# Kernel optimization log

Measured on AMD Instinct MI355X. Metric: run time of the kernel, lower is better.

Reference implementation:

```python
import jax, jax.numpy as jnp
import numpy as np

B, LQ, LK, D, H = 4, 2048, 2048, 1024, 16
HD = D // H  # head dim = 64


def setup_inputs() -> dict:
    key = jax.random.key(0)
    ks = jax.random.split(key, 8)
    s = 1.0 / np.sqrt(D)
    return {
        "zt": jax.random.normal(ks[0], (B, LQ, D), jnp.float32),
        "ic": jax.random.normal(ks[1], (B, LK, D), jnp.float32),
        "Wq": jax.random.normal(ks[2], (D, D), jnp.float32) * s,
        "bq": jax.random.normal(ks[3], (D,), jnp.float32) * 0.01,
        "Wk": jax.random.normal(ks[4], (D, D), jnp.float32) * s,
        "bk": jax.random.normal(ks[5], (D,), jnp.float32) * 0.01,
        "Wv": jax.random.normal(ks[6], (D, D), jnp.float32) * s,
        "bv": jax.random.normal(ks[7], (D,), jnp.float32) * 0.01,
    }


def reference(zt, ic, Wq, bq, Wk, bk, Wv, bv):
    # Linear projections (torch Linear: x @ W.T + b); weights here stored as [out, in]
    q = zt @ Wq.T + bq            # [B, LQ, D]
    k = ic @ Wk.T + bk            # [B, LK, D]
    v = ic @ Wv.T + bv            # [B, LK, D]
    # split heads -> [B, H, L, HD]
    q = q.reshape(B, LQ, H, HD).transpose(0, 2, 1, 3)
    k = k.reshape(B, LK, H, HD).transpose(0, 2, 1, 3)
    v = v.reshape(B, LK, H, HD).transpose(0, 2, 1, 3)
    scale = 1.0 / jnp.sqrt(jnp.asarray(HD, q.dtype))
    scores = jnp.einsum('bhqd,bhkd->bhqk', q, k) * scale  # [B, H, LQ, LK]
    attn = jax.nn.softmax(scores, axis=-1)
    out = jnp.einsum('bhqk,bhkd->bhqd', attn, v)          # [B, H, LQ, HD]
    return out.transpose(0, 2, 1, 3).reshape(B, LQ, D)
```

## Files before the change

kernel.cpp:

```cpp
#include <hip/hip_runtime.h>
#include <hip/hip_bf16.h>
#include <cstdint>

#define B_  4
#define LQ_ 2048
#define LK_ 2048
#define D_  1024
#define H_  16
#define HD_ 64

typedef __attribute__((ext_vector_type(8))) short bf16x8;
typedef __attribute__((ext_vector_type(4))) float f32x4;

#if defined(__has_builtin)
#if __has_builtin(__builtin_amdgcn_exp2f)
#define EXP2F(x) __builtin_amdgcn_exp2f(x)
#else
#define EXP2F(x) exp2f(x)
#endif
#else
#define EXP2F(x) exp2f(x)
#endif

__device__ __forceinline__ unsigned short f2b(float f) {
    union { float f; unsigned u; } v; v.f = f;
    unsigned u = v.u;
    unsigned r = (u + 0x7fffu + ((u >> 16) & 1u)) >> 16;
    return (unsigned short)r;
}

__device__ __forceinline__ void gl_lds16(const unsigned short* g, unsigned short* l) {
    __builtin_amdgcn_global_load_lds(
        (const __attribute__((address_space(1))) unsigned int*)(g),
        (__attribute__((address_space(3))) unsigned int*)(l),
        16, 0, 0);
}

#define PHASE_BARRIER() do { \
    __builtin_amdgcn_sched_barrier(0); \
    __builtin_amdgcn_s_barrier(); \
    __builtin_amdgcn_sched_barrier(0); } while (0)

#define WAITVM(N) do { \
    asm volatile("s_waitcnt vmcnt(" #N ")" ::: "memory"); \
    __builtin_amdgcn_sched_barrier(0); } while (0)

__global__ void cvt_all(const float* __restrict__ a0, unsigned short* __restrict__ d0,
                        const float* __restrict__ a1, unsigned short* __restrict__ d1,
                        const float* __restrict__ w0, unsigned short* __restrict__ e0, float s0,
                        const float* __restrict__ w1, unsigned short* __restrict__ e1,
                        const float* __restrict__ w2, unsigned short* __restrict__ e2,
                        int nact, int nw) {
    const float* in; unsigned short* out; float s = 1.0f; int n;
    switch (blockIdx.y) {
        case 0: in = a0; out = d0; n = nact; break;
        case 1: in = a1; out = d1; n = nact; break;
        case 2: in = w0; out = e0; n = nw; s = s0; break;
        case 3: in = w1; out = e1; n = nw; break;
        default: in = w2; out = e2; n = nw; break;
    }
    int i = (blockIdx.x * blockDim.x + threadIdx.x) * 8;
    int stride = gridDim.x * blockDim.x * 8;
    for (; i < n; i += stride) {
        float4 x = *(const float4*)(in + i);
        float4 y = *(const float4*)(in + i + 4);
        bf16x8 v;
        v[0] = (short)f2b(x.x * s); v[1] = (short)f2b(x.y * s);
        v[2] = (short)f2b(x.z * s); v[3] = (short)f2b(x.w * s);
        v[4] = (short)f2b(y.x * s); v[5] = (short)f2b(y.y * s);
        v[6] = (short)f2b(y.z * s); v[7] = (short)f2b(y.w * s);
        *(bf16x8*)(out + i) = v;
    }
}

__global__ __launch_bounds__(512, 2) void qkv_gemm(
    const unsigned short* __restrict__ Xq,
    const unsigned short* __restrict__ Xkv,
    const unsigned short* __restrict__ Wqb, const unsigned short* __restrict__ Wkb,
    const unsigned short* __restrict__ Wvb,
    const float* __restrict__ bq, const float* __restrict__ bk,
    const float* __restrict__ bv, float qscale,
    unsigned short* __restrict__ Qb, unsigned short* __restrict__ Kb,
    unsigned short* __restrict__ Vtb)
{
    __shared__ unsigned short AS[4][8192];
    __shared__ unsigned short BS[4][8192];

    const int proj = blockIdx.y >> 2;
    const int nt0  = blockIdx.y & 3;
    const unsigned short* X = (proj == 0) ? Xq : Xkv;
    const unsigned short* W = (proj == 0) ? Wqb : (proj == 1 ? Wkb : Wvb);
    const float* bias       = (proj == 0) ? bq  : (proj == 1 ? bk  : bv);
    const float bscale      = (proj == 0) ? qscale : 1.0f;

    const int tid  = threadIdx.x;
    const int lane = tid & 63;
    const int w    = tid >> 6;
    const int wm   = w & 1, wn = w >> 1;
    const int m0   = blockIdx.x * 256;
    const int n0   = nt0 * 256;
    const int l15  = lane & 15, quad = lane >> 4;

    f32x4 acc[8][4] = {};

    const unsigned short* gA0 = X + (size_t)(m0 + (w * 2) * 16 + l15) * 1024 + quad * 8;
    const unsigned short* gA1 = gA0 + 16 * 1024;
    const unsigned short* gB0 = W + (size_t)(n0 + (w * 2) * 16 + l15) * 1024 + quad * 8;
    const unsigned short* gB1 = gB0 + 16 * 1024;

#define STAGE_A(slot, koff) do { \
    gl_lds16(gA0 + (koff), &AS[slot][(w * 2) * 512 + lane * 8]); \
    gl_lds16(gA1 + (koff), &AS[slot][(w * 2 + 1) * 512 + lane * 8]); } while (0)
#define STAGE_B(slot, koff) do { \
    gl_lds16(gB0 + (koff), &BS[slot][(w * 2) * 512 + lane * 8]); \
    gl_lds16(gB1 + (koff), &BS[slot][(w * 2 + 1) * 512 + lane * 8]); } while (0)

    const int aoff = (wm * 8) * 512 + lane * 8;
    const int boff = (wn * 4) * 512 + lane * 8;

    STAGE_A(0, 0);   STAGE_B(0, 0);
    STAGE_A(1, 32);  STAGE_B(1, 32);
    STAGE_A(2, 64);  STAGE_B(2, 64);
    WAITVM(8);
    __builtin_amdgcn_s_barrier();
    __builtin_amdgcn_sched_barrier(0);

    #pragma unroll 2
    for (int t = 0; t < 16; ++t) {
        const int s0 = (2 * t) & 3;
        const int s1 = (2 * t + 1) & 3;
        const int s3 = (2 * t + 3) & 3;

        bf16x8 af[8], bf0, bf1;

        #pragma unroll
        for (int i = 0; i < 8; ++i)
            af[i] = *(const bf16x8*)(&AS[s0][aoff + i * 512]);
        bf0 = *(const bf16x8*)(&BS[s0][boff]);
        bf1 = *(const bf16x8*)(&BS[s0][boff + 512]);
        PHASE_BARRIER();
        __builtin_amdgcn_s_setprio(1);
        #pragma unroll
        for (int i = 0; i < 8; ++i) {
            acc[i][0] = __builtin_amdgcn_mfma_f32_16x16x32_bf16(af[i], bf0, acc[i][0], 0, 0, 0);
            acc[i][1] = __builtin_amdgcn_mfma_f32_16x16x32_bf16(af[i], bf1, acc[i][1], 0, 0, 0);
        }
        __builtin_amdgcn_s_setprio(0);
        if (t < 15) STAGE_A(s3, (t + 1) * 64 + 32);

        bf0 = *(const bf16x8*)(&BS[s0][boff + 1024]);
        bf1 = *(const bf16x8*)(&BS[s0][boff + 1536]);
        if (t < 14) { WAITVM(6); } else { WAITVM(0); }
        PHASE_BARRIER();
        __builtin_amdgcn_s_setprio(1);
        #pragma unroll
        for (int i = 0; i < 8; ++i) {
            acc[i][2] = __builtin_amdgcn_mfma_f32_16x16x32_bf16(af[i], bf0, acc[i][2], 0, 0, 0);
            acc[i][3] = __builtin_amdgcn_mfma_f32_16x16x32_bf16(af[i], bf1, acc[i][3], 0, 0, 0);
        }
        __builtin_amdgcn_s_setprio(0);
        if (t < 15) STAGE_B(s3, (t + 1) * 64 + 32);

        #pragma unroll
        for (int i = 0; i < 8; ++i)
            af[i] = *(const bf16x8*)(&AS[s1][aoff + i * 512]);
        bf0 = *(const bf16x8*)(&BS[s1][boff]);
        bf1 = *(const bf16x8*)(&BS[s1][boff + 512]);
        PHASE_BARRIER();
        __builtin_amdgcn_s_setprio(1);
        #pragma unroll
        for (int i = 0; i < 8; ++i) {
            acc[i][0] = __builtin_amdgcn_mfma_f32_16x16x32_bf16(af[i], bf0, acc[i][0], 0, 0, 0);
            acc[i][1] = __builtin_amdgcn_mfma_f32_16x16x32_bf16(af[i], bf1, acc[i][1], 0, 0, 0);
        }
        __builtin_amdgcn_s_setprio(0);
        if (t < 14) STAGE_A(s0, (t + 2) * 64);

        bf0 = *(const bf16x8*)(&BS[s1][boff + 1024]);
        bf1 = *(const bf16x8*)(&BS[s1][boff + 1536]);
        if (t < 14) { WAITVM(6); } else if (t == 14) { WAITVM(4); }
        PHASE_BARRIER();
        __builtin_amdgcn_s_setprio(1);
        #pragma unroll
        for (int i = 0; i < 8; ++i) {
            acc[i][2] = __builtin_amdgcn_mfma_f32_16x16x32_bf16(af[i], bf0, acc[i][2], 0, 0, 0);
            acc[i][3] = __builtin_amdgcn_mfma_f32_16x16x32_bf16(af[i], bf1, acc[i][3], 0, 0, 0);
        }
        __builtin_amdgcn_s_setprio(0);
        if (t < 14) STAGE_B(s0, (t + 2) * 64);
    }

#undef STAGE_A
#undef STAGE_B

    float bvv[4];
    #pragma unroll
    for (int j = 0; j < 4; ++j)
        bvv[j] = bias[n0 + wn * 64 + j * 16 + l15] * bscale;

    if (proj == 2) {
        #pragma unroll
        for (int i = 0; i < 8; ++i) {
            int row = m0 + wm * 128 + i * 16 + quad * 4;
            int bb  = row >> 11;
            int tt  = row & 2047;
            #pragma unroll
            for (int j = 0; j < 4; ++j) {
                int col = n0 + wn * 64 + j * 16 + l15;
                unsigned s0v = f2b(acc[i][j][0] + bvv[j]);
                unsigned s1v = f2b(acc[i][j][1] + bvv[j]);
                unsigned s2v = f2b(acc[i][j][2] + bvv[j]);
                unsigned s3v = f2b(acc[i][j][3] + bvv[j]);
                uint2 pk;
                pk.x = s0v | (s1v << 16);
                pk.y = s2v | (s3v << 16);
                *(uint2*)(Vtb + ((size_t)(bb * 1024 + col)) * 2048 + tt) = pk;
            }
        }
    } else {
        unsigned short* Y = (proj == 0) ? Qb : Kb;
        #pragma unroll
        for (int i = 0; i < 8; ++i) {
            #pragma unroll
            for (int r = 0; r < 4; ++r) {
                int row = m0 + wm * 128 + i * 16 + quad * 4 + r;
                unsigned short* yp = Y + (size_t)row * 1024 + n0 + wn * 64;
                #pragma unroll
                for (int j = 0; j < 4; ++j)
                    yp[j * 16 + l15] = f2b(acc[i][j][r] + bvv[j]);
            }
        }
    }
}

__global__ __launch_bounds__(256, 2) void attn_kernel(
    const unsigned short* __restrict__ Q,
    const unsigned short* __restrict__ Kp,
    const unsigned short* __restrict__ Vt,
    float* __restrict__ Out)
{
    __shared__ unsigned short Ks[2][16 * 512];
    __shared__ unsigned short Vs[16 * 512];
    __shared__ unsigned short Ps[4][4096];

    const int tid  = threadIdx.x;
    const int lane = tid & 63;
    const int w    = tid >> 6;
    const int l15  = lane & 15, quad = lane >> 4;

    const int bid = blockIdx.x + (blockIdx.y << 3) + (blockIdx.z << 7);
    const int glo = bid & 7;
    const int jx  = bid >> 3;
    const int qt  = jx & 7;
    const int g   = glo + ((jx >> 3) << 3);
    const int h   = g & 15;
    const int b   = g >> 4;

    bf16x8 qf[4][2];
    #pragma unroll
    for (int half = 0; half < 4; ++half) {
        const unsigned short* qptr =
            Q + (size_t)(b * LQ_ + qt * 256 + w * 64 + half * 16 + l15) * 1024 + h * 64;
        qf[half][0] = *(const bf16x8*)(qptr + quad * 8);
        qf[half][1] = *(const bf16x8*)(qptr + 32 + quad * 8);
    }

    bf16x8 ones;
    #pragma unroll
    for (int j = 0; j < 8; ++j) ones[j] = (short)0x3F80;

    f32x4 oacc[4][4] = {};
    f32x4 lacc[4]    = {};

    const unsigned short* Kbase = Kp + (size_t)b * LK_ * 1024 + h * 64;
    const unsigned short* Vbase = Vt + (size_t)(b * 16 + h) * 64 * 2048;

    const unsigned short* gK[4];
    unsigned short* lK[4];
    const unsigned short* gV[4];
    unsigned short* lV[4];
    #pragma unroll
    for (int j = 0; j < 4; ++j) {
        int kt = w + (j >> 1) * 4, dblk = j & 1;
        gK[j] = Kbase + (size_t)(kt * 16 + l15) * 1024 + dblk * 32 + quad * 8;
        lK[j] = &Ks[0][(kt * 2 + dblk) * 512 + lane * 8];
        gV[j] = Vbase + (size_t)(w * 16 + l15) * 2048 + j * 32 + quad * 8;
        lV[j] = &Vs[(w * 4 + j) * 512 + lane * 8];
    }

    const int pws = (quad >> 1) * 128 + l15 * 8 + (quad & 1) * 4;
    unsigned short* PwB = &Ps[w][pws];
    const unsigned short* PrB = &Ps[w][lane * 8];
    const unsigned short* KfrB = &Ks[0][lane * 8];
    const unsigned short* Vfr = &Vs[lane * 8];

    #pragma unroll
    for (int j = 0; j < 4; ++j) gl_lds16(gK[j], lK[j]);

    for (int t = 0; t < 16; ++t) {
        const int cur = t & 1;
        const int k0 = t * 128;

        #pragma unroll
        for (int j = 0; j < 4; ++j) gl_lds16(gV[j] + k0, lV[j]);
        if (t < 15) {
            const int stoff = (cur ^ 1) * 8192;
            #pragma unroll
            for (int j = 0; j < 4; ++j)
                gl_lds16(gK[j] + (size_t)(t + 1) * (128 * 1024), lK[j] + stoff);
        }
        if (t == 0) {
            WAITVM(8);
            PHASE_BARRIER();
        }
        const unsigned short* Kfr = KfrB + cur * 8192;

        #pragma unroll
        for (int cc = 0; cc < 2; ++cc) {
            f32x4 st[4][4] = {};
            #pragma unroll
            for (int ti = 0; ti < 4; ++ti)
                #pragma unroll
                for (int dblk = 0; dblk < 2; ++dblk) {
                    bf16x8 kf = *(const bf16x8*)(Kfr + ((cc * 4 + ti) * 2 + dblk) * 512);
                    #pragma unroll
                    for (int half = 0; half < 4; ++half)
                        st[half][ti] = __builtin_amdgcn_mfma_f32_16x16x32_bf16(
                            kf, qf[half][dblk], st[half][ti], 0, 0, 0);
                }

            #pragma unroll
            for (int half = 0; half < 4; ++half) {
                unsigned short* pw = PwB + half * 1024;
                #pragma unroll
                for (int ti = 0; ti < 4; ++ti) {
                    unsigned u0 = __float_as_uint(EXP2F(st[half][ti][0])) + 0x8000u;
                    unsigned u1 = __float_as_uint(EXP2F(st[half][ti][1])) + 0x8000u;
                    unsigned u2 = __float_as_uint(EXP2F(st[half][ti][2])) + 0x8000u;
                    unsigned u3 = __float_as_uint(EXP2F(st[half][ti][3])) + 0x8000u;
                    uint2 pk;
                    pk.x = __builtin_amdgcn_perm(u1, u0, 0x07060302);
                    pk.y = __builtin_amdgcn_perm(u3, u2, 0x07060302);
                    *(uint2*)(pw + ti * 256) = pk;
                }
            }

            if (cc == 0) {
                if (t < 15) { WAITVM(4); } else { WAITVM(0); }
                PHASE_BARRIER();
            }

            #pragma unroll
            for (int hbl = 0; hbl < 2; ++hbl) {
                bf16x8 pf[4];
                #pragma unroll
                for (int half = 0; half < 4; ++half) {
                    pf[half] = *(const bf16x8*)(PrB + half * 1024 + hbl * 512);
                    lacc[half] = __builtin_amdgcn_mfma_f32_16x16x32_bf16(
                        pf[half], ones, lacc[half], 0, 0, 0);
                }
                int hb = cc * 2 + hbl;
                #pragma unroll
                for (int nt = 0; nt < 4; ++nt) {
                    bf16x8 vf = *(const bf16x8*)(Vfr + (nt * 4 + hb) * 512);
                    #pragma unroll
                    for (int half = 0; half < 4; ++half)
                        oacc[half][nt] = __builtin_amdgcn_mfma_f32_16x16x32_bf16(
                            pf[half], vf, oacc[half][nt], 0, 0, 0);
                }
            }
        }

        if (t < 15) {
            WAITVM(0);
            PHASE_BARRIER();
        }
    }

    #pragma unroll
    for (int half = 0; half < 4; ++half) {
        float il[4];
        #pragma unroll
        for (int r = 0; r < 4; ++r) il[r] = 1.0f / lacc[half][r];
        #pragma unroll
        for (int nt = 0; nt < 4; ++nt) {
            #pragma unroll
            for (int r = 0; r < 4; ++r) {
                size_t orow = (size_t)(b * LQ_ + qt * 256 + w * 64 + half * 16 + quad * 4 + r);
                Out[orow * 1024 + h * 64 + nt * 16 + l15] = oacc[half][nt][r] * il[r];
            }
        }
    }
}

extern "C" void kernel_launch(void* const* d_in, const int* in_sizes, int n_in,
                              void* d_out, int out_size, void* d_ws, size_t ws_size,
                              hipStream_t stream) {
    const float* zt = (const float*)d_in[0];
    const float* ic = (const float*)d_in[1];
    const float* Wq = (const float*)d_in[2];
    const float* bq = (const float*)d_in[3];
    const float* Wk = (const float*)d_in[4];
    const float* bk = (const float*)d_in[5];
    const float* Wv = (const float*)d_in[6];
    const float* bv = (const float*)d_in[7];
    float* out = (float*)d_out;

    const size_t M8 = (size_t)8192 * 1024;
    const size_t M1 = (size_t)1024 * 1024;
    unsigned short* Qb  = (unsigned short*)d_ws;
    unsigned short* Kb  = Qb  + M8;
    unsigned short* Vtb = Kb  + M8;
    unsigned short* Xz  = Vtb + M8;
    unsigned short* Xi  = Xz  + M8;
    unsigned short* Wqb = Xi  + M8;
    unsigned short* Wkb = Wqb + M1;
    unsigned short* Wvb = Wkb + M1;

    const float qscale = 0.125f * 1.44269504088896f;

    dim3 gcv(4096, 5);
    cvt_all<<<gcv, 256, 0, stream>>>(zt, Xz, ic, Xi,
                                     Wq, Wqb, qscale, Wk, Wkb, Wv, Wvb,
                                     (int)M8, (int)M1);

    dim3 gproj(32, 12);
    qkv_gemm<<<gproj, 512, 0, stream>>>(Xz, Xi, Wqb, Wkb, Wvb,
                                        bq, bk, bv, qscale, Qb, Kb, Vtb);

    dim3 gattn(8, 16, 4);
    attn_kernel<<<gattn, 256, 0, stream>>>(Qb, Kb, Vtb, out);
}
```

Baseline: 289.9 us.

## Load K directly into registers and double-buffer V in LDS for attention

The attention kernel stops staging K through shared memory. Each wave now loads its K fragments straight from global memory into registers, using a two-stage register prefetch (kf0/kf1) across half-tiles. V becomes double-buffered in LDS, there are fewer barriers per tile, and MFMA sections get raised wave priority. The change aims to cut LDS traffic and synchronisation stalls, at the cost of more registers and uncoalesced per-wave K reads. The conversion kernel's grid is also cut from 4096 to 512 blocks in x, which assumes cvt_all loops over its range with a grid stride.

```diff
diff --git a/kernel.cpp b/kernel.cpp
--- a/kernel.cpp
+++ b/kernel.cpp
@@ -239,8 +239,7 @@
     const unsigned short* __restrict__ Vt,
     float* __restrict__ Out)
 {
-    __shared__ unsigned short Ks[2][16 * 512];
-    __shared__ unsigned short Vs[16 * 512];
+    __shared__ unsigned short Vs[2][16 * 512];
     __shared__ unsigned short Ps[4][4096];
 
     const int tid  = threadIdx.x;
@@ -264,6 +263,7 @@
         qf[half][0] = *(const bf16x8*)(qptr + quad * 8);
         qf[half][1] = *(const bf16x8*)(qptr + 32 + quad * 8);
     }
+    WAITVM(0);
 
     bf16x8 ones;
     #pragma unroll
@@ -275,105 +275,159 @@
     const unsigned short* Kbase = Kp + (size_t)b * LK_ * 1024 + h * 64;
     const unsigned short* Vbase = Vt + (size_t)(b * 16 + h) * 64 * 2048;
 
-    const unsigned short* gK[4];
-    unsigned short* lK[4];
+    const unsigned short* gKl = Kbase + (size_t)l15 * 1024 + quad * 8;
+
     const unsigned short* gV[4];
     unsigned short* lV[4];
     #pragma unroll
     for (int j = 0; j < 4; ++j) {
-        int kt = w + (j >> 1) * 4, dblk = j & 1;
-        gK[j] = Kbase + (size_t)(kt * 16 + l15) * 1024 + dblk * 32 + quad * 8;
-        lK[j] = &Ks[0][(kt * 2 + dblk) * 512 + lane * 8];
         gV[j] = Vbase + (size_t)(w * 16 + l15) * 2048 + j * 32 + quad * 8;
-        lV[j] = &Vs[(w * 4 + j) * 512 + lane * 8];
+        lV[j] = &Vs[0][(w * 4 + j) * 512 + lane * 8];
     }
 
     const int pws = (quad >> 1) * 128 + l15 * 8 + (quad & 1) * 4;
     unsigned short* PwB = &Ps[w][pws];
     const unsigned short* PrB = &Ps[w][lane * 8];
-    const unsigned short* KfrB = &Ks[0][lane * 8];
-    const unsigned short* Vfr = &Vs[lane * 8];
-
-    #pragma unroll
-    for (int j = 0; j < 4; ++j) gl_lds16(gK[j], lK[j]);
+    const unsigned short* VfrB = &Vs[0][lane * 8];
+
+    bf16x8 kf0[8], kf1[8];
+
+    #pragma unroll
+    for (int j = 0; j < 4; ++j) gl_lds16(gV[j], lV[j]);
+    __builtin_amdgcn_sched_barrier(0);
+    #pragma unroll
+    for (int j = 0; j < 8; ++j)
+        kf0[j] = *(const bf16x8*)(gKl + (size_t)((j >> 1) * 16) * 1024 + (j & 1) * 32);
+    __builtin_amdgcn_sched_barrier(0);
 
     for (int t = 0; t < 16; ++t) {
-        const int cur = t & 1;
+        const int p  = t & 1;
         const int k0 = t * 128;
 
-        #pragma unroll
-        for (int j = 0; j < 4; ++j) gl_lds16(gV[j] + k0, lV[j]);
+        WAITVM(8);
+        PHASE_BARRIER();
+
+        #pragma unroll
+        for (int j = 0; j < 8; ++j)
+            kf1[j] = *(const bf16x8*)(gKl + (size_t)(k0 + 64 + (j >> 1) * 16) * 1024 + (j & 1) * 32);
+        __builtin_amdgcn_sched_barrier(0);
+
+        WAITVM(8);
+
+        const unsigned short* Vfr = VfrB + p * 8192;
+
+        f32x4 st[4][4] = {};
+        __builtin_amdgcn_s_setprio(1);
+        #pragma unroll
+        for (int ti = 0; ti < 4; ++ti)
+            #pragma unroll
+            for (int dblk = 0; dblk < 2; ++dblk)
+                #pragma unroll
+                for (int half = 0; half < 4; ++half)
+                    st[half][ti] = __builtin_amdgcn_mfma_f32_16x16x32_bf16(
+                        kf0[ti * 2 + dblk], qf[half][dblk], st[half][ti], 0, 0, 0);
+        __builtin_amdgcn_s_setprio(0);
+
         if (t < 15) {
-            const int stoff = (cur ^ 1) * 8192;
             #pragma unroll
             for (int j = 0; j < 4; ++j)
-                gl_lds16(gK[j] + (size_t)(t + 1) * (128 * 1024), lK[j] + stoff);
-        }
-        if (t == 0) {
-            WAITVM(8);
-            PHASE_BARRIER();
-        }
-        const unsigned short* Kfr = KfrB + cur * 8192;
-
-        #pragma unroll
-        for (int cc = 0; cc < 2; ++cc) {
-            f32x4 st[4][4] = {};
-            #pragma unroll
-            for (int ti = 0; ti < 4; ++ti)
+                gl_lds16(gV[j] + k0 + 128, lV[j] + (p ^ 1) * 8192);
+            __builtin_amdgcn_sched_barrier(0);
+        }
+
+        #pragma unroll
+        for (int half = 0; half < 4; ++half) {
+            unsigned short* pw = PwB + half * 1024;
+            #pragma unroll
+            for (int ti = 0; ti < 4; ++ti) {
+                unsigned u0 = __float_as_uint(EXP2F(st[half][ti][0])) + 0x8000u;
+                unsigned u1 = __float_as_uint(EXP2F(st[half][ti][1])) + 0x8000u;
+                unsigned u2 = __float_as_uint(EXP2F(st[half][ti][2])) + 0x8000u;
+                unsigned u3 = __float_as_uint(EXP2F(st[half][ti][3])) + 0x8000u;
+                uint2 pk;
+                pk.x = __builtin_amdgcn_perm(u1, u0, 0x07060302);
+                pk.y = __builtin_amdgcn_perm(u3, u2, 0x07060302);
+                *(uint2*)(pw + ti * 256) = pk;
+            }
+        }
+
+        #pragma unroll
+        for (int hbl = 0; hbl < 2; ++hbl) {
+            bf16x8 pf[4];
+            __builtin_amdgcn_s_setprio(1);
+            #pragma unroll
+            for (int half = 0; half < 4; ++half) {
+                pf[half] = *(const bf16x8*)(PrB + half * 1024 + hbl * 512);
+                lacc[half] = __builtin_amdgcn_mfma_f32_16x16x32_bf16(
+                    pf[half], ones, lacc[half], 0, 0, 0);
+            }
+            #pragma unroll
+            for (int nt = 0; nt < 4; ++nt) {
+                bf16x8 vf = *(const bf16x8*)(Vfr + (nt * 4 + hbl) * 512);
                 #pragma unroll
-                for (int dblk = 0; dblk < 2; ++dblk) {
-                    bf16x8 kf = *(const bf16x8*)(Kfr + ((cc * 4 + ti) * 2 + dblk) * 512);
-                    #pragma unroll
-                    for (int half = 0; half < 4; ++half)
-                        st[half][ti] = __builtin_amdgcn_mfma_f32_16x16x32_bf16(
-                            kf, qf[half][dblk], st[half][ti], 0, 0, 0);
-                }
-
+                for (int half = 0; half < 4; ++half)
+                    oacc[half][nt] = __builtin_amdgcn_mfma_f32_16x16x32_bf16(
+                        pf[half], vf, oacc[half][nt], 0, 0, 0);
+            }
+            __builtin_amdgcn_s_setprio(0);
+        }
+
+        if (t < 15) { WAITVM(4); } else { WAITVM(0); }
+
+        f32x4 su[4][4] = {};
+        __builtin_amdgcn_s_setprio(1);
+        #pragma unroll
+        for (int ti = 0; ti < 4; ++ti)
+            #pragma unroll
+            for (int dblk = 0; dblk < 2; ++dblk)
+                #pragma unroll
+                for (int half = 0; half < 4; ++half)
+                    su[half][ti] = __builtin_amdgcn_mfma_f32_16x16x32_bf16(
+                        kf1[ti * 2 + dblk], qf[half][dblk], su[half][ti], 0, 0, 0);
+        __builtin_amdgcn_s_setprio(0);
+
+        if (t < 15) {
+            #pragma unroll
+            for (int j = 0; j < 8; ++j)
+                kf0[j] = *(const bf16x8*)(gKl + (size_t)(k0 + 128 + (j >> 1) * 16) * 1024 + (j & 1) * 32);
+            __builtin_amdgcn_sched_barrier(0);
+        }
+
+        #pragma unroll
+        for (int half = 0; half < 4; ++half) {
+            unsigned short* pw = PwB + half * 1024;
+            #pragma unroll
+            for (int ti = 0; ti < 4; ++ti) {
+                unsigned u0 = __float_as_uint(EXP2F(su[half][ti][0])) + 0x8000u;
+                unsigned u1 = __float_as_uint(EXP2F(su[half][ti][1])) + 0x8000u;
+                unsigned u2 = __float_as_uint(EXP2F(su[half][ti][2])) + 0x8000u;
+                unsigned u3 = __float_as_uint(EXP2F(su[half][ti][3])) + 0x8000u;
+                uint2 pk;
+                pk.x = __builtin_amdgcn_perm(u1, u0, 0x07060302);
+                pk.y = __builtin_amdgcn_perm(u3, u2, 0x07060302);
+                *(uint2*)(pw + ti * 256) = pk;
+            }
+        }
+
+        #pragma unroll
+        for (int hbl = 0; hbl < 2; ++hbl) {
+            bf16x8 pf[4];
+            __builtin_amdgcn_s_setprio(1);
             #pragma unroll
             for (int half = 0; half < 4; ++half) {
-                unsigned short* pw = PwB + half * 1024;
+                pf[half] = *(const bf16x8*)(PrB + half * 1024 + hbl * 512);
+                lacc[half] = __builtin_amdgcn_mfma_f32_16x16x32_bf16(
+                    pf[half], ones, lacc[half], 0, 0, 0);
+            }
+            #pragma unroll
+            for (int nt = 0; nt < 4; ++nt) {
+                bf16x8 vf = *(const bf16x8*)(Vfr + (nt * 4 + 2 + hbl) * 512);
                 #pragma unroll
-                for (int ti = 0; ti < 4; ++ti) {
-                    unsigned u0 = __float_as_uint(EXP2F(st[half][ti][0])) + 0x8000u;
-                    unsigned u1 = __float_as_uint(EXP2F(st[half][ti][1])) + 0x8000u;
-                    unsigned u2 = __float_as_uint(EXP2F(st[half][ti][2])) + 0x8000u;
-                    unsigned u3 = __float_as_uint(EXP2F(st[half][ti][3])) + 0x8000u;
-                    uint2 pk;
-                    pk.x = __builtin_amdgcn_perm(u1, u0, 0x07060302);
-                    pk.y = __builtin_amdgcn_perm(u3, u2, 0x07060302);
-                    *(uint2*)(pw + ti * 256) = pk;
-                }
-            }
-
-            if (cc == 0) {
-                if (t < 15) { WAITVM(4); } else { WAITVM(0); }
-                PHASE_BARRIER();
-            }
-
-            #pragma unroll
-            for (int hbl = 0; hbl < 2; ++hbl) {
-                bf16x8 pf[4];
-                #pragma unroll
-                for (int half = 0; half < 4; ++half) {
-                    pf[half] = *(const bf16x8*)(PrB + half * 1024 + hbl * 512);
-                    lacc[half] = __builtin_amdgcn_mfma_f32_16x16x32_bf16(
-                        pf[half], ones, lacc[half], 0, 0, 0);
-                }
-                int hb = cc * 2 + hbl;
-                #pragma unroll
-                for (int nt = 0; nt < 4; ++nt) {
-                    bf16x8 vf = *(const bf16x8*)(Vfr + (nt * 4 + hb) * 512);
-                    #pragma unroll
-                    for (int half = 0; half < 4; ++half)
-                        oacc[half][nt] = __builtin_amdgcn_mfma_f32_16x16x32_bf16(
-                            pf[half], vf, oacc[half][nt], 0, 0, 0);
-                }
-            }
-        }
-
-        if (t < 15) {
-            WAITVM(0);
-            PHASE_BARRIER();
+                for (int half = 0; half < 4; ++half)
+                    oacc[half][nt] = __builtin_amdgcn_mfma_f32_16x16x32_bf16(
+                        pf[half], vf, oacc[half][nt], 0, 0, 0);
+            }
+            __builtin_amdgcn_s_setprio(0);
         }
     }
 
@@ -419,7 +473,7 @@
 
     const float qscale = 0.125f * 1.44269504088896f;
 
-    dim3 gcv(4096, 5);
+    dim3 gcv(512, 5);
     cvt_all<<<gcv, 256, 0, stream>>>(zt, Xz, ic, Xi,
                                      Wq, Wqb, qscale, Wk, Wkb, Wv, Wvb,
                                      (int)M8, (int)M1);
```

New measurement: 320.9 us. 10.7% more time.

## Halve QKV GEMM LDS ring to double buffer and raise occupancy bound

Applied to the files above, without the earlier changes.

Shrinks the LDS staging ring for the QKV projection GEMM from four slots to two and restructures the main loop as a simple double-buffered pipeline. Both A and B are staged together after each slot is consumed, with an lgkmcnt wait before the barrier. The launch bound goes from 2 to 4 blocks per CU to fit more resident workgroups. The trade-off is a shallower prefetch distance and tighter register limits, since 4x512 threads per CU caps VGPRs and 128 accumulator floats per thread may spill.

```diff
diff --git a/kernel.cpp b/kernel.cpp
--- a/kernel.cpp
+++ b/kernel.cpp
@@ -43,6 +43,10 @@
 
 #define WAITVM(N) do { \
     asm volatile("s_waitcnt vmcnt(" #N ")" ::: "memory"); \
+    __builtin_amdgcn_sched_barrier(0); } while (0)
+
+#define WAITLGKM0() do { \
+    asm volatile("s_waitcnt lgkmcnt(0)" ::: "memory"); \
     __builtin_amdgcn_sched_barrier(0); } while (0)
 
 __global__ void cvt_all(const float* __restrict__ a0, unsigned short* __restrict__ d0,
@@ -73,7 +77,7 @@
     }
 }
 
-__global__ __launch_bounds__(512, 2) void qkv_gemm(
+__global__ __launch_bounds__(512, 4) void qkv_gemm(
     const unsigned short* __restrict__ Xq,
     const unsigned short* __restrict__ Xkv,
     const unsigned short* __restrict__ Wqb, const unsigned short* __restrict__ Wkb,
@@ -83,8 +87,8 @@
     unsigned short* __restrict__ Qb, unsigned short* __restrict__ Kb,
     unsigned short* __restrict__ Vtb)
 {
-    __shared__ unsigned short AS[4][8192];
-    __shared__ unsigned short BS[4][8192];
+    __shared__ unsigned short AS[2][8192];
+    __shared__ unsigned short BS[2][8192];
 
     const int proj = blockIdx.y >> 2;
     const int nt0  = blockIdx.y & 3;
@@ -120,74 +124,68 @@
 
     STAGE_A(0, 0);   STAGE_B(0, 0);
     STAGE_A(1, 32);  STAGE_B(1, 32);
-    STAGE_A(2, 64);  STAGE_B(2, 64);
-    WAITVM(8);
-    __builtin_amdgcn_s_barrier();
-    __builtin_amdgcn_sched_barrier(0);
-
-    #pragma unroll 2
+
     for (int t = 0; t < 16; ++t) {
-        const int s0 = (2 * t) & 3;
-        const int s1 = (2 * t + 1) & 3;
-        const int s3 = (2 * t + 3) & 3;
-
-        bf16x8 af[8], bf0, bf1;
+        const int ke = t * 64;
+
+        WAITVM(4);
+        PHASE_BARRIER();
+
+        bf16x8 af[8], b0, b1, b2, b3;
 
         #pragma unroll
         for (int i = 0; i < 8; ++i)
-            af[i] = *(const bf16x8*)(&AS[s0][aoff + i * 512]);
-        bf0 = *(const bf16x8*)(&BS[s0][boff]);
-        bf1 = *(const bf16x8*)(&BS[s0][boff + 512]);
+            af[i] = *(const bf16x8*)(&AS[0][aoff + i * 512]);
+        b0 = *(const bf16x8*)(&BS[0][boff]);
+        b1 = *(const bf16x8*)(&BS[0][boff + 512]);
+        b2 = *(const bf16x8*)(&BS[0][boff + 1024]);
+        b3 = *(const bf16x8*)(&BS[0][boff + 1536]);
+        __builtin_amdgcn_s_setprio(1);
+        #pragma unroll
+        for (int i = 0; i < 8; ++i) {
+            acc[i][0] = __builtin_amdgcn_mfma_f32_16x16x32_bf16(af[i], b0, acc[i][0], 0, 0, 0);
+            acc[i][1] = __builtin_amdgcn_mfma_f32_16x16x32_bf16(af[i], b1, acc[i][1], 0, 0, 0);
+        }
+        __builtin_amdgcn_s_setprio(0);
+
+        WAITLGKM0();
         PHASE_BARRIER();
         __builtin_amdgcn_s_setprio(1);
         #pragma unroll
         for (int i = 0; i < 8; ++i) {
-            acc[i][0] = __builtin_amdgcn_mfma_f32_16x16x32_bf16(af[i], bf0, acc[i][0], 0, 0, 0);
-            acc[i][1] = __builtin_amdgcn_mfma_f32_16x16x32_bf16(af[i], bf1, acc[i][1], 0, 0, 0);
+            acc[i][2] = __builtin_amdgcn_mfma_f32_16x16x32_bf16(af[i], b2, acc[i][2], 0, 0, 0);
+            acc[i][3] = __builtin_amdgcn_mfma_f32_16x16x32_bf16(af[i], b3, acc[i][3], 0, 0, 0);
         }
         __builtin_amdgcn_s_setprio(0);
-        if (t < 15) STAGE_A(s3, (t + 1) * 64 + 32);
-
-        bf0 = *(const bf16x8*)(&BS[s0][boff + 1024]);
-        bf1 = *(const bf16x8*)(&BS[s0][boff + 1536]);
-        if (t < 14) { WAITVM(6); } else { WAITVM(0); }
+        if (t < 15) { STAGE_A(0, ke + 64); STAGE_B(0, ke + 64); }
+
+        if (t < 15) { WAITVM(4); } else { WAITVM(0); }
+        PHASE_BARRIER();
+        #pragma unroll
+        for (int i = 0; i < 8; ++i)
+            af[i] = *(const bf16x8*)(&AS[1][aoff + i * 512]);
+        b0 = *(const bf16x8*)(&BS[1][boff]);
+        b1 = *(const bf16x8*)(&BS[1][boff + 512]);
+        b2 = *(const bf16x8*)(&BS[1][boff + 1024]);
+        b3 = *(const bf16x8*)(&BS[1][boff + 1536]);
+        __builtin_amdgcn_s_setprio(1);
+        #pragma unroll
+        for (int i = 0; i < 8; ++i) {
+            acc[i][0] = __builtin_amdgcn_mfma_f32_16x16x32_bf16(af[i], b0, acc[i][0], 0, 0, 0);
+            acc[i][1] = __builtin_amdgcn_mfma_f32_16x16x32_bf16(af[i], b1, acc[i][1], 0, 0, 0);
+        }
+        __builtin_amdgcn_s_setprio(0);
+
+        WAITLGKM0();
         PHASE_BARRIER();
         __builtin_amdgcn_s_setprio(1);
         #pragma unroll
         for (int i = 0; i < 8; ++i) {
-            acc[i][2] = __builtin_amdgcn_mfma_f32_16x16x32_bf16(af[i], bf0, acc[i][2], 0, 0, 0);
-            acc[i][3] = __builtin_amdgcn_mfma_f32_16x16x32_bf16(af[i], bf1, acc[i][3], 0, 0, 0);
+            acc[i][2] = __builtin_amdgcn_mfma_f32_16x16x32_bf16(af[i], b2, acc[i][2], 0, 0, 0);
+            acc[i][3] = __builtin_amdgcn_mfma_f32_16x16x32_bf16(af[i], b3, acc[i][3], 0, 0, 0);
         }
         __builtin_amdgcn_s_setprio(0);
-        if (t < 15) STAGE_B(s3, (t + 1) * 64 + 32);
-
-        #pragma unroll
-        for (int i = 0; i < 8; ++i)
-            af[i] = *(const bf16x8*)(&AS[s1][aoff + i * 512]);
-        bf0 = *(const bf16x8*)(&BS[s1][boff]);
-        bf1 = *(const bf16x8*)(&BS[s1][boff + 512]);
-        PHASE_BARRIER();
-        __builtin_amdgcn_s_setprio(1);
-        #pragma unroll
-        for (int i = 0; i < 8; ++i) {
-            acc[i][0] = __builtin_amdgcn_mfma_f32_16x16x32_bf16(af[i], bf0, acc[i][0], 0, 0, 0);
-            acc[i][1] = __builtin_amdgcn_mfma_f32_16x16x32_bf16(af[i], bf1, acc[i][1], 0, 0, 0);
-        }
-        __builtin_amdgcn_s_setprio(0);
-        if (t < 14) STAGE_A(s0, (t + 2) * 64);
-
-        bf0 = *(const bf16x8*)(&BS[s1][boff + 1024]);
-        bf1 = *(const bf16x8*)(&BS[s1][boff + 1536]);
-        if (t < 14) { WAITVM(6); } else if (t == 14) { WAITVM(4); }
-        PHASE_BARRIER();
-        __builtin_amdgcn_s_setprio(1);
-        #pragma unroll
-        for (int i = 0; i < 8; ++i) {
-            acc[i][2] = __builtin_amdgcn_mfma_f32_16x16x32_bf16(af[i], bf0, acc[i][2], 0, 0, 0);
-            acc[i][3] = __builtin_amdgcn_mfma_f32_16x16x32_bf16(af[i], bf1, acc[i][3], 0, 0, 0);
-        }
-        __builtin_amdgcn_s_setprio(0);
-        if (t < 14) STAGE_B(s0, (t + 2) * 64);
+        if (t < 15) { STAGE_A(1, ke + 96); STAGE_B(1, ke + 96); }
     }
 
 #undef STAGE_A
```

After: 796.1 us. +174.6%, slower.

## Shrink QKV GEMM N-tile to 128 and simplify pipeline into uniform phases

Applied to the files above, without the earlier changes.

The QKV projection GEMM tile changes from 256x256 to 256x128, doubling the grid to 768 blocks. The main loop is restructured into a uniform QPHASE macro that waits, barriers, loads fragments and issues MFMAs, then stages A and B together. This gives more blocks for better CU occupancy and balance, and halves the accumulator registers and LDS. In exchange there is less reuse of A per block (more global traffic for X) and more barriers per unit of compute.

```diff
diff --git a/kernel.cpp b/kernel.cpp
--- a/kernel.cpp
+++ b/kernel.cpp
@@ -83,11 +83,11 @@
     unsigned short* __restrict__ Qb, unsigned short* __restrict__ Kb,
     unsigned short* __restrict__ Vtb)
 {
-    __shared__ unsigned short AS[4][8192];
-    __shared__ unsigned short BS[4][8192];
-
-    const int proj = blockIdx.y >> 2;
-    const int nt0  = blockIdx.y & 3;
+    __shared__ unsigned short AS[4][16 * 512];
+    __shared__ unsigned short BS[4][8 * 512];
+
+    const int proj = blockIdx.y >> 3;
+    const int nt0  = blockIdx.y & 7;
     const unsigned short* X = (proj == 0) ? Xq : Xkv;
     const unsigned short* W = (proj == 0) ? Wqb : (proj == 1 ? Wkb : Wvb);
     const float* bias       = (proj == 0) ? bq  : (proj == 1 ? bk  : bv);
@@ -98,105 +98,71 @@
     const int w    = tid >> 6;
     const int wm   = w & 1, wn = w >> 1;
     const int m0   = blockIdx.x * 256;
-    const int n0   = nt0 * 256;
+    const int n0   = nt0 * 128;
     const int l15  = lane & 15, quad = lane >> 4;
 
-    f32x4 acc[8][4] = {};
+    f32x4 acc[8][2] = {};
 
     const unsigned short* gA0 = X + (size_t)(m0 + (w * 2) * 16 + l15) * 1024 + quad * 8;
     const unsigned short* gA1 = gA0 + 16 * 1024;
-    const unsigned short* gB0 = W + (size_t)(n0 + (w * 2) * 16 + l15) * 1024 + quad * 8;
-    const unsigned short* gB1 = gB0 + 16 * 1024;
-
-#define STAGE_A(slot, koff) do { \
+    const unsigned short* gB0 = W + (size_t)(n0 + w * 16 + l15) * 1024 + quad * 8;
+
+#define STAGE(slot, koff) do { \
     gl_lds16(gA0 + (koff), &AS[slot][(w * 2) * 512 + lane * 8]); \
-    gl_lds16(gA1 + (koff), &AS[slot][(w * 2 + 1) * 512 + lane * 8]); } while (0)
-#define STAGE_B(slot, koff) do { \
-    gl_lds16(gB0 + (koff), &BS[slot][(w * 2) * 512 + lane * 8]); \
-    gl_lds16(gB1 + (koff), &BS[slot][(w * 2 + 1) * 512 + lane * 8]); } while (0)
+    gl_lds16(gA1 + (koff), &AS[slot][(w * 2 + 1) * 512 + lane * 8]); \
+    gl_lds16(gB0 + (koff), &BS[slot][w * 512 + lane * 8]); } while (0)
 
     const int aoff = (wm * 8) * 512 + lane * 8;
-    const int boff = (wn * 4) * 512 + lane * 8;
-
-    STAGE_A(0, 0);   STAGE_B(0, 0);
-    STAGE_A(1, 32);  STAGE_B(1, 32);
-    STAGE_A(2, 64);  STAGE_B(2, 64);
-    WAITVM(8);
-    __builtin_amdgcn_s_barrier();
-    __builtin_amdgcn_sched_barrier(0);
+    const int boff = (wn * 2) * 512 + lane * 8;
+
+    STAGE(0, 0);
+    STAGE(1, 32);
+    STAGE(2, 64);
+
+#define QPHASE(slot, WN, do_stage, sslot, skoff) do { \
+    WAITVM(WN); \
+    PHASE_BARRIER(); \
+    bf16x8 af[8], b0, b1; \
+    _Pragma("unroll") \
+    for (int i = 0; i < 8; ++i) \
+        af[i] = *(const bf16x8*)(&AS[slot][aoff + i * 512]); \
+    b0 = *(const bf16x8*)(&BS[slot][boff]); \
+    b1 = *(const bf16x8*)(&BS[slot][boff + 512]); \
+    __builtin_amdgcn_s_setprio(1); \
+    _Pragma("unroll") \
+    for (int i = 0; i < 8; ++i) { \
+        acc[i][0] = __builtin_amdgcn_mfma_f32_16x16x32_bf16(af[i], b0, acc[i][0], 0, 0, 0); \
+        acc[i][1] = __builtin_amdgcn_mfma_f32_16x16x32_bf16(af[i], b1, acc[i][1], 0, 0, 0); \
+    } \
+    __builtin_amdgcn_s_setprio(0); \
+    if (do_stage) STAGE(sslot, skoff); } while (0)
 
     #pragma unroll 2
     for (int t = 0; t < 16; ++t) {
         const int s0 = (2 * t) & 3;
         const int s1 = (2 * t + 1) & 3;
-        const int s3 = (2 * t + 3) & 3;
-
-        bf16x8 af[8], bf0, bf1;
-
-        #pragma unroll
-        for (int i = 0; i < 8; ++i)
-            af[i] = *(const bf16x8*)(&AS[s0][aoff + i * 512]);
-        bf0 = *(const bf16x8*)(&BS[s0][boff]);
-        bf1 = *(const bf16x8*)(&BS[s0][boff + 512]);
-        PHASE_BARRIER();
-        __builtin_amdgcn_s_setprio(1);
-        #pragma unroll
-        for (int i = 0; i < 8; ++i) {
-            acc[i][0] = __builtin_amdgcn_mfma_f32_16x16x32_bf16(af[i], bf0, acc[i][0], 0, 0, 0);
-            acc[i][1] = __builtin_amdgcn_mfma_f32_16x16x32_bf16(af[i], bf1, acc[i][1], 0, 0, 0);
-        }
-        __builtin_amdgcn_s_setprio(0);
-        if (t < 15) STAGE_A(s3, (t + 1) * 64 + 32);
-
-        bf0 = *(const bf16x8*)(&BS[s0][boff + 1024]);
-        bf1 = *(const bf16x8*)(&BS[s0][boff + 1536]);
-        if (t < 14) { WAITVM(6); } else { WAITVM(0); }
-        PHASE_BARRIER();
-        __builtin_amdgcn_s_setprio(1);
-        #pragma unroll
-        for (int i = 0; i < 8; ++i) {
-            acc[i][2] = __builtin_amdgcn_mfma_f32_16x16x32_bf16(af[i], bf0, acc[i][2], 0, 0, 0);
-            acc[i][3] = __builtin_amdgcn_mfma_f32_16x16x32_bf16(af[i], bf1, acc[i][3], 0, 0, 0);
-        }
-        __builtin_amdgcn_s_setprio(0);
-        if (t < 15) STAGE_B(s3, (t + 1) * 64 + 32);
-
-        #pragma unroll
-        for (int i = 0; i < 8; ++i)
-            af[i] = *(const bf16x8*)(&AS[s1][aoff + i * 512]);
-        bf0 = *(const bf16x8*)(&BS[s1][boff]);
-        bf1 = *(const bf16x8*)(&BS[s1][boff + 512]);
-        PHASE_BARRIER();
-        __builtin_amdgcn_s_setprio(1);
-        #pragma unroll
-        for (int i = 0; i < 8; ++i) {
-            acc[i][0] = __builtin_amdgcn_mfma_f32_16x16x32_bf16(af[i], bf0, acc[i][0], 0, 0, 0);
-            acc[i][1] = __builtin_amdgcn_mfma_f32_16x16x32_bf16(af[i], bf1, acc[i][1], 0, 0, 0);
-        }
-        __builtin_amdgcn_s_setprio(0);
-        if (t < 14) STAGE_A(s0, (t + 2) * 64);
-
-        bf0 = *(const bf16x8*)(&BS[s1][boff + 1024]);
-        bf1 = *(const bf16x8*)(&BS[s1][boff + 1536]);
-        if (t < 14) { WAITVM(6); } else if (t == 14) { WAITVM(4); }
-        PHASE_BARRIER();
-        __builtin_amdgcn_s_setprio(1);
-        #pragma unroll
-        for (int i = 0; i < 8; ++i) {
-            acc[i][2] = __builtin_amdgcn_mfma_f32_16x16x32_bf16(af[i], bf0, acc[i][2], 0, 0, 0);
-            acc[i][3] = __builtin_amdgcn_mfma_f32_16x16x32_bf16(af[i], bf1, acc[i][3], 0, 0, 0);
-        }
-        __builtin_amdgcn_s_setprio(0);
-        if (t < 14) STAGE_B(s0, (t + 2) * 64);
-    }
-
-#undef STAGE_A
-#undef STAGE_B
-
-    float bvv[4];
-    #pragma unroll
-    for (int j = 0; j < 4; ++j)
-        bvv[j] = bias[n0 + wn * 64 + j * 16 + l15] * bscale;
+        const int sa = (2 * t + 3) & 3;
+        const int sb = (2 * t + 4) & 3;
+
+        if (t < 15) {
+            QPHASE(s0, 6, 1, sa, (2 * t + 3) * 32);
+        } else {
+            QPHASE(s0, 3, 0, sa, 0);
+        }
+        if (t < 15) {
+            QPHASE(s1, 6, (t <= 13), sb, (2 * t + 4) * 32);
+        } else {
+            QPHASE(s1, 0, 0, sb, 0);
+        }
+    }
+
+#undef QPHASE
+#undef STAGE
+
+    float bvv[2];
+    #pragma unroll
+    for (int j = 0; j < 2; ++j)
+        bvv[j] = bias[n0 + wn * 32 + j * 16 + l15] * bscale;
 
     if (proj == 2) {
         #pragma unroll
@@ -205,8 +171,8 @@
             int bb  = row >> 11;
             int tt  = row & 2047;
             #pragma unroll
-            for (int j = 0; j < 4; ++j) {
-                int col = n0 + wn * 64 + j * 16 + l15;
+            for (int j = 0; j < 2; ++j) {
+                int col = n0 + wn * 32 + j * 16 + l15;
                 unsigned s0v = f2b(acc[i][j][0] + bvv[j]);
                 unsigned s1v = f2b(acc[i][j][1] + bvv[j]);
                 unsigned s2v = f2b(acc[i][j][2] + bvv[j]);
@@ -224,9 +190,9 @@
             #pragma unroll
             for (int r = 0; r < 4; ++r) {
                 int row = m0 + wm * 128 + i * 16 + quad * 4 + r;
-                unsigned short* yp = Y + (size_t)row * 1024 + n0 + wn * 64;
-                #pragma unroll
-                for (int j = 0; j < 4; ++j)
+                unsigned short* yp = Y + (size_t)row * 1024 + n0 + wn * 32;
+                #pragma unroll
+                for (int j = 0; j < 2; ++j)
                     yp[j * 16 + l15] = f2b(acc[i][j][r] + bvv[j]);
             }
         }
@@ -424,7 +390,7 @@
                                      Wq, Wqb, qscale, Wk, Wkb, Wv, Wvb,
                                      (int)M8, (int)M1);
 
-    dim3 gproj(32, 12);
+    dim3 gproj(32, 24);
     qkv_gemm<<<gproj, 512, 0, stream>>>(Xz, Xi, Wqb, Wkb, Wvb,
                                         bq, bk, bv, qscale, Qb, Kb, Vtb);
 
```

After: 284.6 us. No clear change (-1.8%).
